# Performance work log

Measured on AMD Instinct MI355X. Metric: run time of the kernel, lower is better.

The kernel has to match this reference:

```python
import jax, jax.numpy as jnp
import numpy as np

EPS = 1e-5
B, C_IN, T_IN = 512, 12, 5000
NF, HID, LAT = 32, 64, 32


def setup_inputs() -> dict:
    key = jax.random.key(0)
    ks = jax.random.split(key, 12)
    inp = {
        "x": jax.random.normal(ks[0], (B, C_IN, T_IN), dtype=jnp.float32),
        # conv stack
        "conv1_w": jax.random.normal(ks[1], (32, C_IN, 50), dtype=jnp.float32) * 0.05,
        "conv1_b": jnp.zeros((32,), dtype=jnp.float32),
        "bn1_g": jnp.ones((32,), dtype=jnp.float32),
        "bn1_b": jnp.zeros((32,), dtype=jnp.float32),
        "conv2_w": jax.random.normal(ks[2], (NF, 32, 25), dtype=jnp.float32) * 0.05,
        "conv2_b": jnp.zeros((NF,), dtype=jnp.float32),
        "bn2_g": jnp.ones((NF,), dtype=jnp.float32),
        "bn2_b": jnp.zeros((NF,), dtype=jnp.float32),
        # input projection + layernorm
        "proj_w": jax.random.normal(ks[3], (LAT, NF), dtype=jnp.float32) * 0.1,
        "proj_b": jnp.zeros((LAT,), dtype=jnp.float32),
        "ln_g": jnp.ones((LAT,), dtype=jnp.float32),
        "ln_b": jnp.zeros((LAT,), dtype=jnp.float32),
        # PLRNN recurrence params
        "A": jnp.eye(LAT, dtype=jnp.float32) * 0.9,
        "W": jax.random.normal(ks[4], (LAT, HID), dtype=jnp.float32) * 0.1,
        "h_bias": jnp.zeros((HID,), dtype=jnp.float32),
        # output projection
        "out_w": jax.random.normal(ks[5], (LAT, LAT), dtype=jnp.float32) * 0.1,
        "out_b": jnp.zeros((LAT,), dtype=jnp.float32),
    }
    return inp


def _conv1d(x, w, b, stride):
    # x: [B, C, T], w: [O, I, K]
    y = jax.lax.conv_general_dilated(
        x, w, window_strides=(stride,), padding="VALID",
        dimension_numbers=("NCH", "OIH", "NCH"))
    return y + b[None, :, None]


def _batchnorm_train(x, g, b):
    # training-mode BN over (batch, time) per channel; x: [B, C, T]
    mean = jnp.mean(x, axis=(0, 2), keepdims=True)
    var = jnp.mean((x - mean) ** 2, axis=(0, 2), keepdims=True)
    return (x - mean) * jax.lax.rsqrt(var + EPS) * g[None, :, None] + b[None, :, None]


def _layernorm(x, g, b):
    mean = jnp.mean(x, axis=-1, keepdims=True)
    var = jnp.mean((x - mean) ** 2, axis=-1, keepdims=True)
    return (x - mean) * jax.lax.rsqrt(var + EPS) * g + b


def reference(x, conv1_w, conv1_b, bn1_g, bn1_b, conv2_w, conv2_b, bn2_g, bn2_b,
              proj_w, proj_b, ln_g, ln_b, A, W, h_bias, out_w, out_b):
    # conv front-end
    y = jax.nn.relu(_batchnorm_train(_conv1d(x, conv1_w, conv1_b, 10), bn1_g, bn1_b))
    y = jax.nn.relu(_batchnorm_train(_conv1d(y, conv2_w, conv2_b, 5), bn2_g, bn2_b))
    y = jnp.transpose(y, (0, 2, 1))  # [B, T, NF], T = 95

    # input projection + LN, vectorized over all timesteps
    xt = _layernorm(jnp.einsum("btf,lf->btl", y, proj_w) + proj_b, ln_g, ln_b)  # [B, T, L]
    xs = jnp.transpose(xt, (1, 0, 2))  # [T, B, L] for scan

    def step(h, x_t):
        # h: [B, L]
        linear = h @ A.T
        nonlinear = jax.nn.relu(h @ W + h_bias) @ W.T
        h_new = linear + nonlinear + x_t
        return h_new, h_new

    h0 = jnp.zeros((x.shape[0], A.shape[0]), dtype=x.dtype)
    _, outputs = jax.lax.scan(step, h0, xs)  # [T, B, L]

    pooled = jnp.mean(outputs, axis=0)  # [B, L]
    return pooled @ out_w.T + out_b
```

## Files before the change

kernel.cpp:

```cpp
#include <hip/hip_runtime.h>

#define NB    512
#define CIN   12
#define TIN   5000
#define C1    32
#define T1    496
#define T2    95
#define LATD  32
#define HIDD  64

#define OFS_STATS 0
#define OFS_W1P   256
#define OFS_W2P   19456
#define OFS_Y1    45056
#define OFS_Y2    8171520
#define OFS_XS    OFS_Y1

__global__ void prep_kernel(const float* __restrict__ w1, const float* __restrict__ w2,
                            float* __restrict__ ws) {
    int idx = blockIdx.x * 256 + threadIdx.x;
    if (idx < 256) ws[idx] = 0.f;
    int j = idx - 256;
    if (j >= 0 && j < 19200) {
        int ic = j / 1600, r = j % 1600, k = r / 32, oc = r % 32;
        ws[OFS_W1P + j] = w1[oc * 600 + ic * 50 + k];
    }
    int j2 = idx - 19456;
    if (j2 >= 0 && j2 < 25600) {
        int ic = j2 / 800, r = j2 % 800, k = r / 32, oc = r % 32;
        ws[OFS_W2P + j2] = w2[oc * 800 + ic * 25 + k];
    }
}

__global__ __launch_bounds__(256, 4) void conv1_kernel(const float* __restrict__ x,
                                                       const float* __restrict__ b1,
                                                       float* __restrict__ ws) {
    const float* w1p = ws + OFS_W1P;
    float* y1 = ws + OFS_Y1;
    float* stats = ws + OFS_STATS;
    int b  = blockIdx.x >> 1;
    int t0 = (blockIdx.x & 1) * 256;
    int tid = threadIdx.x;
    int ocg = tid & 7, tg = tid >> 3;
    int oc0 = ocg * 4, lt0 = tg * 8;
    int xbase = 82 * tg;

    __shared__ __align__(16) float xs_s[2][2664];
    __shared__ __align__(16) float ws_s[2][1600];
    __shared__ float sred[256];

    float acc[4][8];
#pragma unroll
    for (int a = 0; a < 4; ++a)
#pragma unroll
        for (int c = 0; c < 8; ++c) acc[a][c] = 0.f;

    const float* xb = x + (size_t)b * (CIN * TIN) + t0 * 10;
    int nvalid = TIN - t0 * 10;

    float4 px[3];
    float4 pw[2];

    auto fetch = [&](int ic) {
#pragma unroll
        for (int j = 0; j < 3; ++j) {
            int i = tid + j * 256;
            if (i < 650) {
                int src = 4 * i;
                const float* gp = xb + ic * TIN + src;
                float4 v;
                if (src + 4 <= nvalid) {
                    v = *(const float4*)gp;
                } else {
                    v.x = (src + 0 < nvalid) ? gp[0] : 0.f;
                    v.y = (src + 1 < nvalid) ? gp[1] : 0.f;
                    v.z = (src + 2 < nvalid) ? gp[2] : 0.f;
                    v.w = (src + 3 < nvalid) ? gp[3] : 0.f;
                }
                px[j] = v;
            }
        }
#pragma unroll
        for (int j = 0; j < 2; ++j) {
            int i = tid + j * 256;
            if (i < 400) pw[j] = *(const float4*)(w1p + ic * 1600 + 4 * i);
        }
    };

    fetch(0);
    for (int ic = 0; ic < CIN; ++ic) {
        int cur = ic & 1;
        __syncthreads();
#pragma unroll
        for (int j = 0; j < 3; ++j) {
            int i = tid + j * 256;
            if (i < 650) {
                int src = 4 * i;
                int dst = src + (i / 20) * 2;
                float2 lo; lo.x = px[j].x; lo.y = px[j].y;
                float2 hi; hi.x = px[j].z; hi.y = px[j].w;
                *(float2*)&xs_s[cur][dst]     = lo;
                *(float2*)&xs_s[cur][dst + 2] = hi;
            }
        }
#pragma unroll
        for (int j = 0; j < 2; ++j) {
            int i = tid + j * 256;
            if (i < 400) *(float4*)&ws_s[cur][4 * i] = pw[j];
        }
        if (ic + 1 < CIN) fetch(ic + 1);
        __syncthreads();

#pragma unroll 1
        for (int kp = 0; kp < 25; ++kp) {
            const int k = kp * 2;
            const float* wr = &ws_s[cur][k * 32 + oc0];
            float4 w00 = *(const float4*)wr;
            float4 w10 = *(const float4*)(wr + 32);
            float2 xv[8];
#pragma unroll
            for (int jt = 0; jt < 8; ++jt) {
                int r = jt * 10 + k;
                int ad = xbase + r + ((r >= 80) ? 2 : 0);
                xv[jt] = *(const float2*)&xs_s[cur][ad];
            }
            float wk[4]  = {w00.x, w00.y, w00.z, w00.w};
            float wk1[4] = {w10.x, w10.y, w10.z, w10.w};
#pragma unroll
            for (int jo = 0; jo < 4; ++jo)
#pragma unroll
                for (int jt = 0; jt < 8; ++jt)
                    acc[jo][jt] = fmaf(wk1[jo], xv[jt].y, fmaf(wk[jo], xv[jt].x, acc[jo][jt]));
        }
    }

    float bias[4];
#pragma unroll
    for (int jo = 0; jo < 4; ++jo) bias[jo] = b1[oc0 + jo];

    bool tvalid = (t0 + lt0) <= (T1 - 8);
    float psum[4], psq[4];
#pragma unroll
    for (int jo = 0; jo < 4; ++jo) {
        float s = 0.f, q = 0.f;
        if (tvalid) {
            float tmp[8];
#pragma unroll
            for (int jt = 0; jt < 8; ++jt) {
                float v = acc[jo][jt] + bias[jo];
                tmp[jt] = v; s += v; q = fmaf(v, v, q);
            }
            float* yrow = y1 + (size_t)(b * 32 + oc0 + jo) * T1 + t0 + lt0;
            float4 o0; o0.x = tmp[0]; o0.y = tmp[1]; o0.z = tmp[2]; o0.w = tmp[3];
            float4 o1; o1.x = tmp[4]; o1.y = tmp[5]; o1.z = tmp[6]; o1.w = tmp[7];
            *(float4*)yrow       = o0;
            *(float4*)(yrow + 4) = o1;
        }
        psum[jo] = s; psq[jo] = q;
    }
#pragma unroll
    for (int off = 32; off >= 8; off >>= 1) {
#pragma unroll
        for (int jo = 0; jo < 4; ++jo) {
            psum[jo] += __shfl_down(psum[jo], off, 64);
            psq[jo]  += __shfl_down(psq[jo],  off, 64);
        }
    }
    int lane = tid & 63, wvi = tid >> 6;
    if (lane < 8) {
#pragma unroll
        for (int jo = 0; jo < 4; ++jo) {
            sred[((wvi * 8 + lane) * 4 + jo) * 2 + 0] = psum[jo];
            sred[((wvi * 8 + lane) * 4 + jo) * 2 + 1] = psq[jo];
        }
    }
    __syncthreads();
    if (tid < 64) {
        int oc = tid >> 1, which = tid & 1;
        int og = oc >> 2, jo = oc & 3;
        float v = 0.f;
#pragma unroll
        for (int w = 0; w < 4; ++w)
            v += sred[((w * 8 + og) * 4 + jo) * 2 + which];
        atomicAdd(&stats[which * 32 + oc], v);
    }
}

__global__ __launch_bounds__(192, 2) void conv2_kernel(const float* __restrict__ b2,
                                                       const float* __restrict__ g1,
                                                       const float* __restrict__ be1,
                                                       float* __restrict__ ws) {
    const float* w2p = ws + OFS_W2P;
    const float* y1 = ws + OFS_Y1;
    float* y2 = ws + OFS_Y2;
    float* stats = ws + OFS_STATS;
    int b = blockIdx.x;
    int tid = threadIdx.x;
    int ocg = tid & 7, tg = tid >> 3;
    int oc0 = ocg * 4, lt0 = tg * 4;

    __shared__ __align__(16) float a1s[2][500];
    __shared__ __align__(16) float w2s[2][800];
    __shared__ float sred[192];
    __shared__ float bns[64];

    if (tid < 32) {
        float mean = stats[tid] * (1.f / 253952.f);
        float var  = stats[32 + tid] * (1.f / 253952.f) - mean * mean;
        float s = g1[tid] * rsqrtf(var + 1e-5f);
        bns[tid]      = s;
        bns[32 + tid] = be1[tid] - mean * s;
    }

    float acc[4][4];
#pragma unroll
    for (int a = 0; a < 4; ++a)
#pragma unroll
        for (int c = 0; c < 4; ++c) acc[a][c] = 0.f;

    float4 py, pw0, pw1;
    auto fetch = [&](int ic) {
        const float* yrow = y1 + (size_t)(b * 32 + ic) * T1;
        if (tid < 124) py = *(const float4*)(yrow + 4 * tid);
        pw0 = *(const float4*)(w2p + ic * 800 + 4 * tid);
        if (tid < 8) pw1 = *(const float4*)(w2p + ic * 800 + 4 * (tid + 192));
    };

    fetch(0);
    for (int ic = 0; ic < 32; ++ic) {
        int cur = ic & 1;
        __syncthreads();
        if (tid < 124) {
            float s1 = bns[ic], sh1 = bns[32 + ic];
            float4 v = py;
            v.x = fmaxf(fmaf(v.x, s1, sh1), 0.f);
            v.y = fmaxf(fmaf(v.y, s1, sh1), 0.f);
            v.z = fmaxf(fmaf(v.z, s1, sh1), 0.f);
            v.w = fmaxf(fmaf(v.w, s1, sh1), 0.f);
            *(float4*)&a1s[cur][4 * tid] = v;
        }
        *(float4*)&w2s[cur][4 * tid] = pw0;
        if (tid < 8) *(float4*)&w2s[cur][4 * (tid + 192)] = pw1;
        if (ic + 1 < 32) fetch(ic + 1);
        __syncthreads();

#pragma unroll 1
        for (int kp = 0; kp < 12; ++kp) {
            const int k = kp * 2;
            float4 wA = *(const float4*)&w2s[cur][k * 32 + oc0];
            float4 wB = *(const float4*)&w2s[cur][(k + 1) * 32 + oc0];
            float x0[4], x1[4];
#pragma unroll
            for (int jt = 0; jt < 4; ++jt) {
                int a = 20 * tg + 5 * jt + k;
                x0[jt] = a1s[cur][a]; x1[jt] = a1s[cur][a + 1];
            }
            float wk[4]  = {wA.x, wA.y, wA.z, wA.w};
            float wk1[4] = {wB.x, wB.y, wB.z, wB.w};
#pragma unroll
            for (int jo = 0; jo < 4; ++jo)
#pragma unroll
                for (int jt = 0; jt < 4; ++jt)
                    acc[jo][jt] = fmaf(wk1[jo], x1[jt], fmaf(wk[jo], x0[jt], acc[jo][jt]));
        }
        float4 wT = *(const float4*)&w2s[cur][24 * 32 + oc0];
        float wt[4] = {wT.x, wT.y, wT.z, wT.w};
#pragma unroll
        for (int jt = 0; jt < 4; ++jt) {
            float xt_ = a1s[cur][20 * tg + 5 * jt + 24];
#pragma unroll
            for (int jo = 0; jo < 4; ++jo) acc[jo][jt] = fmaf(wt[jo], xt_, acc[jo][jt]);
        }
    }

    float bias[4];
#pragma unroll
    for (int jo = 0; jo < 4; ++jo) bias[jo] = b2[oc0 + jo];

    float psum[4], psq[4];
#pragma unroll
    for (int jo = 0; jo < 4; ++jo) {
        float s = 0.f, q = 0.f;
#pragma unroll
        for (int jt = 0; jt < 4; ++jt) {
            int t2 = lt0 + jt;
            if (t2 < T2) {
                float v = acc[jo][jt] + bias[jo];
                y2[(size_t)(b * 32 + oc0 + jo) * T2 + t2] = v;
                s += v; q = fmaf(v, v, q);
            }
        }
        psum[jo] = s; psq[jo] = q;
    }
#pragma unroll
    for (int off = 32; off >= 8; off >>= 1) {
#pragma unroll
        for (int jo = 0; jo < 4; ++jo) {
            psum[jo] += __shfl_down(psum[jo], off, 64);
            psq[jo]  += __shfl_down(psq[jo],  off, 64);
        }
    }
    int lane = tid & 63, wvi = tid >> 6;
    if (lane < 8) {
#pragma unroll
        for (int jo = 0; jo < 4; ++jo) {
            sred[((wvi * 8 + lane) * 4 + jo) * 2 + 0] = psum[jo];
            sred[((wvi * 8 + lane) * 4 + jo) * 2 + 1] = psq[jo];
        }
    }
    __syncthreads();
    if (tid < 64) {
        int oc = tid >> 1, which = tid & 1;
        int og = oc >> 2, jo = oc & 3;
        float v = 0.f;
#pragma unroll
        for (int w = 0; w < 3; ++w)
            v += sred[((w * 8 + og) * 4 + jo) * 2 + which];
        atomicAdd(&stats[64 + which * 32 + oc], v);
    }
}

__global__ __launch_bounds__(256, 2) void proj_kernel(const float* __restrict__ g2,
                                                      const float* __restrict__ be2,
                                                      const float* __restrict__ pw,
                                                      const float* __restrict__ pb,
                                                      const float* __restrict__ lng,
                                                      const float* __restrict__ lnb,
                                                      float* __restrict__ ws) {
    int b = blockIdx.x;
    int tid = threadIdx.x;
    __shared__ float a2s[3040];
    __shared__ float pws[1056];
    __shared__ float bns2[64];
    const float* stats = ws + OFS_STATS;
    const float* y2 = ws + OFS_Y2 + (size_t)b * (32 * T2);
    float* xsg = ws + OFS_XS;

    if (tid < 32) {
        float mean = stats[64 + tid] * (1.f / 48640.f);
        float var  = stats[96 + tid] * (1.f / 48640.f) - mean * mean;
        float s = g2[tid] * rsqrtf(var + 1e-5f);
        bns2[tid]      = s;
        bns2[32 + tid] = be2[tid] - mean * s;
    }
    __syncthreads();

    for (int f = 0; f < 32; ++f) {
        float s2  = bns2[f];
        float sh2 = bns2[32 + f];
        if (tid < T2)
            a2s[f * T2 + tid] = fmaxf(fmaf(y2[f * T2 + tid], s2, sh2), 0.f);
    }
    for (int i = tid; i < 1024; i += 256)
        pws[(i >> 5) * 33 + (i & 31)] = pw[i];

    int l = tid & 31, ts = tid >> 5;
    float pbv = pb[l], lg = lng[l], lb = lnb[l];
    __syncthreads();

    for (int it = 0; it < 12; ++it) {
        int t = ts + 8 * it;
        if (t < T2) {
            float v = pbv;
#pragma unroll
            for (int f = 0; f < 32; ++f)
                v = fmaf(a2s[f * T2 + t], pws[l * 33 + f], v);
            float sum = v;
#pragma unroll
            for (int off = 16; off >= 1; off >>= 1) sum += __shfl_xor(sum, off, 64);
            float mean = sum * (1.f / 32.f);
            float d = v - mean;
            float q = d * d;
#pragma unroll
            for (int off = 16; off >= 1; off >>= 1) q += __shfl_xor(q, off, 64);
            float o = d * rsqrtf(q * (1.f / 32.f) + 1e-5f) * lg + lb;
            xsg[(size_t)t * (NB * 32) + b * 32 + l] = o;
        }
    }
}

__global__ __launch_bounds__(64)
__attribute__((amdgpu_waves_per_eu(1, 1)))
void scan_kernel(const float* __restrict__ Am,
                 const float* __restrict__ Wm,
                 const float* __restrict__ hbp,
                 const float* __restrict__ ow,
                 const float* __restrict__ ob,
                 const float* __restrict__ ws,
                 float* __restrict__ out) {
    int b = blockIdx.x;
    int lane = threadIdx.x;
    int l = lane & 31, half = lane >> 5;
    __shared__ __align__(16) float hs[32];
    __shared__ __align__(16) float hds[64];
    __shared__ float ows[1056];

    float Wc[32], WT[32], Ah[16];
#pragma unroll
    for (int j = 0; j < 32; ++j) Wc[j] = Wm[j * HIDD + lane];
#pragma unroll
    for (int m = 0; m < 32; ++m) WT[m] = Wm[l * HIDD + half * 32 + m];
#pragma unroll
    for (int j = 0; j < 16; ++j) Ah[j] = Am[l * 32 + half * 16 + j];
    float hbv = hbp[lane];
    for (int i = lane; i < 1024; i += 64)
        ows[(i >> 5) * 33 + (i & 31)] = ow[i];

    const float* xsg = ws + OFS_XS + b * 32;
    if (lane < 32) hs[l] = 0.f;
    float xv = xsg[l];
    float pool = 0.f;
    __syncthreads();

    for (int t = 0; t < T2; ++t) {
        __syncthreads();
        float4 hv[8];
#pragma unroll
        for (int q = 0; q < 8; ++q) hv[q] = *(const float4*)&hs[4 * q];
        float a0 = hbv, a1 = 0.f, a2 = 0.f, a3 = 0.f;
#pragma unroll
        for (int q = 0; q < 8; ++q) {
            a0 = fmaf(Wc[4 * q + 0], hv[q].x, a0);
            a1 = fmaf(Wc[4 * q + 1], hv[q].y, a1);
            a2 = fmaf(Wc[4 * q + 2], hv[q].z, a2);
            a3 = fmaf(Wc[4 * q + 3], hv[q].w, a3);
        }
        float hid = fmaxf((a0 + a1) + (a2 + a3), 0.f);
        float4 hl[4];
#pragma unroll
        for (int q = 0; q < 4; ++q) hl[q] = *(const float4*)&hs[half * 16 + 4 * q];
        float l0 = 0.f, l1 = 0.f;
#pragma unroll
        for (int q = 0; q < 4; ++q) {
            l0 = fmaf(Ah[4 * q + 0], hl[q].x, l0);
            l1 = fmaf(Ah[4 * q + 1], hl[q].y, l1);
            l0 = fmaf(Ah[4 * q + 2], hl[q].z, l0);
            l1 = fmaf(Ah[4 * q + 3], hl[q].w, l1);
        }
        float lin = l0 + l1;
        hds[lane] = hid;
        __syncthreads();
        float n0 = 0.f, n1 = 0.f, n2 = 0.f, n3 = 0.f;
#pragma unroll
        for (int q = 0; q < 8; ++q) {
            float4 d4 = *(const float4*)&hds[half * 32 + 4 * q];
            n0 = fmaf(WT[4 * q + 0], d4.x, n0);
            n1 = fmaf(WT[4 * q + 1], d4.y, n1);
            n2 = fmaf(WT[4 * q + 2], d4.z, n2);
            n3 = fmaf(WT[4 * q + 3], d4.w, n3);
        }
        float part = (n0 + n1) + (n2 + n3) + lin;
        part += __shfl_xor(part, 32, 64);
        float hnew = part + xv;
        pool += hnew;
        if (t + 1 < T2) xv = xsg[(size_t)(t + 1) * (NB * 32) + l];
        if (lane < 32) hs[l] = hnew;
    }

    __syncthreads();
    if (lane < 32) hs[l] = pool * (1.f / 95.f);
    __syncthreads();
    if (lane < 32) {
        float4 p0 = *(const float4*)&hs[0];
        float4 p1 = *(const float4*)&hs[4];
        float4 p2 = *(const float4*)&hs[8];
        float4 p3 = *(const float4*)&hs[12];
        float4 p4 = *(const float4*)&hs[16];
        float4 p5 = *(const float4*)&hs[20];
        float4 p6 = *(const float4*)&hs[24];
        float4 p7 = *(const float4*)&hs[28];
        float o = ob[l];
        const float* owr = &ows[l * 33];
        o = fmaf(owr[0],  p0.x, o); o = fmaf(owr[1],  p0.y, o);
        o = fmaf(owr[2],  p0.z, o); o = fmaf(owr[3],  p0.w, o);
        o = fmaf(owr[4],  p1.x, o); o = fmaf(owr[5],  p1.y, o);
        o = fmaf(owr[6],  p1.z, o); o = fmaf(owr[7],  p1.w, o);
        o = fmaf(owr[8],  p2.x, o); o = fmaf(owr[9],  p2.y, o);
        o = fmaf(owr[10], p2.z, o); o = fmaf(owr[11], p2.w, o);
        o = fmaf(owr[12], p3.x, o); o = fmaf(owr[13], p3.y, o);
        o = fmaf(owr[14], p3.z, o); o = fmaf(owr[15], p3.w, o);
        o = fmaf(owr[16], p4.x, o); o = fmaf(owr[17], p4.y, o);
        o = fmaf(owr[18], p4.z, o); o = fmaf(owr[19], p4.w, o);
        o = fmaf(owr[20], p5.x, o); o = fmaf(owr[21], p5.y, o);
        o = fmaf(owr[22], p5.z, o); o = fmaf(owr[23], p5.w, o);
        o = fmaf(owr[24], p6.x, o); o = fmaf(owr[25], p6.y, o);
        o = fmaf(owr[26], p6.z, o); o = fmaf(owr[27], p6.w, o);
        o = fmaf(owr[28], p7.x, o); o = fmaf(owr[29], p7.y, o);
        o = fmaf(owr[30], p7.z, o); o = fmaf(owr[31], p7.w, o);
        out[b * 32 + l] = o;
    }
}

extern "C" void kernel_launch(void* const* d_in, const int* in_sizes, int n_in,
                              void* d_out, int out_size, void* d_ws, size_t ws_size,
                              hipStream_t stream) {
    (void)in_sizes; (void)n_in; (void)out_size; (void)ws_size;
    const float* x   = (const float*)d_in[0];
    const float* w1  = (const float*)d_in[1];
    const float* b1  = (const float*)d_in[2];
    const float* g1  = (const float*)d_in[3];
    const float* be1 = (const float*)d_in[4];
    const float* w2  = (const float*)d_in[5];
    const float* b2  = (const float*)d_in[6];
    const float* g2  = (const float*)d_in[7];
    const float* be2 = (const float*)d_in[8];
    const float* pw  = (const float*)d_in[9];
    const float* pb  = (const float*)d_in[10];
    const float* lng = (const float*)d_in[11];
    const float* lnb = (const float*)d_in[12];
    const float* Am  = (const float*)d_in[13];
    const float* Wm  = (const float*)d_in[14];
    const float* hb  = (const float*)d_in[15];
    const float* ow  = (const float*)d_in[16];
    const float* ob  = (const float*)d_in[17];
    float* ws  = (float*)d_ws;
    float* out = (float*)d_out;

    prep_kernel<<<176, 256, 0, stream>>>(w1, w2, ws);
    conv1_kernel<<<1024, 256, 0, stream>>>(x, b1, ws);
    conv2_kernel<<<512, 192, 0, stream>>>(b2, g1, be1, ws);
    proj_kernel<<<512, 256, 0, stream>>>(g2, be2, pw, pb, lng, lnb, ws);
    scan_kernel<<<512, 64, 0, stream>>>(Am, Wm, hb, ow, ob, ws, out);
}
```

Measured before the change: 448.8 us.

## Polyphase-decompose strided conv1/conv2 shared layouts to enable vectorized reuse

Input tiles in shared memory are stored in a stride-phase-major (polyphase) layout, and weights are repacked to match, for both strided convolutions. Each thread then loads contiguous float4 runs per phase and reuses each loaded input across several kernel taps. This cuts the number of LDS reads per FMA and removes the scalar and float2 gathers. In exchange the shared-memory store side becomes scalar scatters, register pressure rises, and the float4 reads at the 268 and 100 row strides may hit bank conflicts.

```diff
diff --git a/kernel.cpp b/kernel.cpp
--- a/kernel.cpp
+++ b/kernel.cpp
@@ -22,13 +22,15 @@
     if (idx < 256) ws[idx] = 0.f;
     int j = idx - 256;
     if (j >= 0 && j < 19200) {
-        int ic = j / 1600, r = j % 1600, k = r / 32, oc = r % 32;
-        ws[OFS_W1P + j] = w1[oc * 600 + ic * 50 + k];
+        int ic = j / 1600, r = j % 1600;
+        int p = r / 160, rr = r % 160, jj = rr / 32, oc = rr % 32;
+        ws[OFS_W1P + j] = w1[oc * 600 + ic * 50 + 10 * jj + p];
     }
     int j2 = idx - 19456;
     if (j2 >= 0 && j2 < 25600) {
-        int ic = j2 / 800, r = j2 % 800, k = r / 32, oc = r % 32;
-        ws[OFS_W2P + j2] = w2[oc * 800 + ic * 25 + k];
+        int ic = j2 / 800, r = j2 % 800;
+        int p = r / 160, rr = r % 160, jj = rr / 32, oc = rr % 32;
+        ws[OFS_W2P + j2] = w2[oc * 800 + ic * 25 + 5 * jj + p];
     }
 }
 
@@ -43,9 +45,8 @@
     int tid = threadIdx.x;
     int ocg = tid & 7, tg = tid >> 3;
     int oc0 = ocg * 4, lt0 = tg * 8;
-    int xbase = 82 * tg;
-
-    __shared__ __align__(16) float xs_s[2][2664];
+
+    __shared__ __align__(16) float xs_s[2][2680];
     __shared__ __align__(16) float ws_s[2][1600];
     __shared__ float sred[256];
 
@@ -95,12 +96,16 @@
         for (int j = 0; j < 3; ++j) {
             int i = tid + j * 256;
             if (i < 650) {
-                int src = 4 * i;
-                int dst = src + (i / 20) * 2;
-                float2 lo; lo.x = px[j].x; lo.y = px[j].y;
-                float2 hi; hi.x = px[j].z; hi.y = px[j].w;
-                *(float2*)&xs_s[cur][dst]     = lo;
-                *(float2*)&xs_s[cur][dst + 2] = hi;
+                int g = 4 * i;
+                int col = g / 10, p = g - 10 * col;
+                float vals[4] = {px[j].x, px[j].y, px[j].z, px[j].w};
+#pragma unroll
+                for (int m = 0; m < 4; ++m) {
+                    int pm = p + m;
+                    int rr = (pm >= 10) ? pm - 10 : pm;
+                    int cc = col + ((pm >= 10) ? 1 : 0);
+                    xs_s[cur][rr * 268 + cc] = vals[m];
+                }
             }
         }
 #pragma unroll
@@ -111,26 +116,35 @@
         if (ic + 1 < CIN) fetch(ic + 1);
         __syncthreads();
 
-#pragma unroll 1
-        for (int kp = 0; kp < 25; ++kp) {
-            const int k = kp * 2;
-            const float* wr = &ws_s[cur][k * 32 + oc0];
-            float4 w00 = *(const float4*)wr;
-            float4 w10 = *(const float4*)(wr + 32);
-            float2 xv[8];
-#pragma unroll
-            for (int jt = 0; jt < 8; ++jt) {
-                int r = jt * 10 + k;
-                int ad = xbase + r + ((r >= 80) ? 2 : 0);
-                xv[jt] = *(const float2*)&xs_s[cur][ad];
-            }
-            float wk[4]  = {w00.x, w00.y, w00.z, w00.w};
-            float wk1[4] = {w10.x, w10.y, w10.z, w10.w};
-#pragma unroll
-            for (int jo = 0; jo < 4; ++jo)
-#pragma unroll
-                for (int jt = 0; jt < 8; ++jt)
-                    acc[jo][jt] = fmaf(wk1[jo], xv[jt].y, fmaf(wk[jo], xv[jt].x, acc[jo][jt]));
+#pragma unroll 2
+        for (int p = 0; p < 10; ++p) {
+            const float* xr = &xs_s[cur][p * 268 + 8 * tg];
+            float4 xa = *(const float4*)(xr);
+            float4 xbv = *(const float4*)(xr + 4);
+            float4 xc = *(const float4*)(xr + 8);
+            float xv[12] = {xa.x, xa.y, xa.z, xa.w,
+                            xbv.x, xbv.y, xbv.z, xbv.w,
+                            xc.x, xc.y, xc.z, xc.w};
+            const float* wr = &ws_s[cur][p * 160 + oc0];
+            float4 w0 = *(const float4*)(wr);
+            float4 w1v = *(const float4*)(wr + 32);
+            float4 w2v = *(const float4*)(wr + 64);
+            float4 w3v = *(const float4*)(wr + 96);
+            float4 w4v = *(const float4*)(wr + 128);
+            float wj[5][4] = {{w0.x, w0.y, w0.z, w0.w},
+                              {w1v.x, w1v.y, w1v.z, w1v.w},
+                              {w2v.x, w2v.y, w2v.z, w2v.w},
+                              {w3v.x, w3v.y, w3v.z, w3v.w},
+                              {w4v.x, w4v.y, w4v.z, w4v.w}};
+#pragma unroll
+            for (int j = 0; j < 5; ++j)
+#pragma unroll
+                for (int jt = 0; jt < 8; ++jt) {
+                    float xx = xv[jt + j];
+#pragma unroll
+                    for (int jo = 0; jo < 4; ++jo)
+                        acc[jo][jt] = fmaf(wj[j][jo], xx, acc[jo][jt]);
+                }
         }
     }
 
@@ -233,43 +247,52 @@
         if (tid < 124) {
             float s1 = bns[ic], sh1 = bns[32 + ic];
             float4 v = py;
-            v.x = fmaxf(fmaf(v.x, s1, sh1), 0.f);
-            v.y = fmaxf(fmaf(v.y, s1, sh1), 0.f);
-            v.z = fmaxf(fmaf(v.z, s1, sh1), 0.f);
-            v.w = fmaxf(fmaf(v.w, s1, sh1), 0.f);
-            *(float4*)&a1s[cur][4 * tid] = v;
+            float vals[4];
+            vals[0] = fmaxf(fmaf(v.x, s1, sh1), 0.f);
+            vals[1] = fmaxf(fmaf(v.y, s1, sh1), 0.f);
+            vals[2] = fmaxf(fmaf(v.z, s1, sh1), 0.f);
+            vals[3] = fmaxf(fmaf(v.w, s1, sh1), 0.f);
+            int g = 4 * tid;
+            int col = g / 5, p = g - 5 * col;
+#pragma unroll
+            for (int m = 0; m < 4; ++m) {
+                int pm = p + m;
+                int rr = (pm >= 5) ? pm - 5 : pm;
+                int cc = col + ((pm >= 5) ? 1 : 0);
+                a1s[cur][rr * 100 + cc] = vals[m];
+            }
         }
         *(float4*)&w2s[cur][4 * tid] = pw0;
         if (tid < 8) *(float4*)&w2s[cur][4 * (tid + 192)] = pw1;
         if (ic + 1 < 32) fetch(ic + 1);
         __syncthreads();
 
-#pragma unroll 1
-        for (int kp = 0; kp < 12; ++kp) {
-            const int k = kp * 2;
-            float4 wA = *(const float4*)&w2s[cur][k * 32 + oc0];
-            float4 wB = *(const float4*)&w2s[cur][(k + 1) * 32 + oc0];
-            float x0[4], x1[4];
-#pragma unroll
-            for (int jt = 0; jt < 4; ++jt) {
-                int a = 20 * tg + 5 * jt + k;
-                x0[jt] = a1s[cur][a]; x1[jt] = a1s[cur][a + 1];
-            }
-            float wk[4]  = {wA.x, wA.y, wA.z, wA.w};
-            float wk1[4] = {wB.x, wB.y, wB.z, wB.w};
-#pragma unroll
-            for (int jo = 0; jo < 4; ++jo)
-#pragma unroll
-                for (int jt = 0; jt < 4; ++jt)
-                    acc[jo][jt] = fmaf(wk1[jo], x1[jt], fmaf(wk[jo], x0[jt], acc[jo][jt]));
-        }
-        float4 wT = *(const float4*)&w2s[cur][24 * 32 + oc0];
-        float wt[4] = {wT.x, wT.y, wT.z, wT.w};
-#pragma unroll
-        for (int jt = 0; jt < 4; ++jt) {
-            float xt_ = a1s[cur][20 * tg + 5 * jt + 24];
-#pragma unroll
-            for (int jo = 0; jo < 4; ++jo) acc[jo][jt] = fmaf(wt[jo], xt_, acc[jo][jt]);
+#pragma unroll 2
+        for (int p = 0; p < 5; ++p) {
+            const float* xr = &a1s[cur][p * 100 + 4 * tg];
+            float4 xa = *(const float4*)(xr);
+            float4 xbv = *(const float4*)(xr + 4);
+            float xv[8] = {xa.x, xa.y, xa.z, xa.w, xbv.x, xbv.y, xbv.z, xbv.w};
+            const float* wr = &w2s[cur][p * 160 + oc0];
+            float4 w0 = *(const float4*)(wr);
+            float4 w1v = *(const float4*)(wr + 32);
+            float4 w2v = *(const float4*)(wr + 64);
+            float4 w3v = *(const float4*)(wr + 96);
+            float4 w4v = *(const float4*)(wr + 128);
+            float wj[5][4] = {{w0.x, w0.y, w0.z, w0.w},
+                              {w1v.x, w1v.y, w1v.z, w1v.w},
+                              {w2v.x, w2v.y, w2v.z, w2v.w},
+                              {w3v.x, w3v.y, w3v.z, w3v.w},
+                              {w4v.x, w4v.y, w4v.z, w4v.w}};
+#pragma unroll
+            for (int j = 0; j < 5; ++j)
+#pragma unroll
+                for (int jt = 0; jt < 4; ++jt) {
+                    float xx = xv[jt + j];
+#pragma unroll
+                    for (int jo = 0; jo < 4; ++jo)
+                        acc[jo][jt] = fmaf(wj[j][jo], xx, acc[jo][jt]);
+                }
         }
     }
 
```

After: 418.7 us. 1.07x faster.
